# Kernel optimization log

Hardware: AMD Instinct MI355X
Metric: run time of the kernel (lower is better)

## Reference

```python
import jax, jax.numpy as jnp
import numpy as np

D_MODEL = 1024
NUM_HEADS = 16
D_K = D_MODEL // NUM_HEADS
B, S = 2, 2048


def setup_inputs() -> dict:
    key = jax.random.key(0)
    ks = jax.random.split(key, 12)
    s = 1.0 / np.sqrt(D_MODEL)
    return {
        "query": jax.random.normal(ks[0], (B, S, D_MODEL), jnp.float32),
        "key": jax.random.normal(ks[1], (B, S, D_MODEL), jnp.float32),
        "value": jax.random.normal(ks[2], (B, S, D_MODEL), jnp.float32),
        "mask": jnp.ones((B, S), jnp.int32),
        "Wq": jax.random.uniform(ks[3], (D_MODEL, D_MODEL), jnp.float32, -s, s),
        "bq": jax.random.uniform(ks[4], (D_MODEL,), jnp.float32, -s, s),
        "Wk": jax.random.uniform(ks[5], (D_MODEL, D_MODEL), jnp.float32, -s, s),
        "bk": jax.random.uniform(ks[6], (D_MODEL,), jnp.float32, -s, s),
        "Wv": jax.random.uniform(ks[7], (D_MODEL, D_MODEL), jnp.float32, -s, s),
        "bv": jax.random.uniform(ks[8], (D_MODEL,), jnp.float32, -s, s),
        "Wo": jax.random.uniform(ks[9], (D_MODEL, D_MODEL), jnp.float32, -s, s),
        "bo": jax.random.uniform(ks[10], (D_MODEL,), jnp.float32, -s, s),
    }


def reference(query, key, value, mask, Wq, bq, Wk, bk, Wv, bv, Wo, bo):
    b, s, _ = query.shape
    scale = jnp.sqrt(jnp.asarray(D_K, jnp.float32)).astype(query.dtype)
    # QKV projections: x @ W.T + b (torch nn.Linear convention)
    Q = (query @ Wq.T + bq).reshape(b, s, NUM_HEADS, D_K).transpose(0, 2, 1, 3)
    K = (key @ Wk.T + bk).reshape(b, -1, NUM_HEADS, D_K).transpose(0, 2, 1, 3)
    V = (value @ Wv.T + bv).reshape(b, -1, NUM_HEADS, D_K).transpose(0, 2, 1, 3)
    # scores in fp32, then cast back to input dtype (matches source)
    scores = jnp.einsum('bhqd,bhkd->bhqk', Q.astype(jnp.float32), K.astype(jnp.float32)) / scale
    scores = scores.astype(Q.dtype)
    # 2D mask [B,S] -> [B,1,1,S], broadcast over heads/queries
    fill = jnp.finfo(scores.dtype).min
    scores = jnp.where(mask[:, None, None, :] == 0, fill, scores)
    attn = jax.nn.softmax(scores, axis=-1)  # dropout p=0 -> identity
    context = jnp.einsum('bhqk,bhkd->bhqd', attn, V)
    context = context.transpose(0, 2, 1, 3).reshape(b, s, D_MODEL)
    return context @ Wo.T + bo
```

## Files before the change

### kernel.cpp

```cpp
#include <hip/hip_runtime.h>


typedef __bf16 bf16_8 __attribute__((ext_vector_type(8)));
typedef float  f32x4  __attribute__((ext_vector_type(4)));

#define MFMA16(a, b, c) __builtin_amdgcn_mfma_f32_16x16x32_bf16((a), (b), (c), 0, 0, 0)

__device__ __forceinline__ void async_ld16(const void* g, void* l) {
  __builtin_amdgcn_global_load_lds(
      (__attribute__((address_space(1))) void*)g,
      (__attribute__((address_space(3))) void*)l, 16, 0, 0);
}

__device__ __forceinline__ void gemm_core_128(
    const __bf16* __restrict__ A, const __bf16* __restrict__ BT, int K,
    int tm, int tn, __bf16* At, __bf16* Bt, f32x4 acc[4][4]) {
  const int tid  = threadIdx.x;
  const int lane = tid & 63;
  const int w    = tid >> 6;
  const int quad = lane >> 4;
  const int c16  = lane & 15;
  const int wm = w >> 1, wn = w & 1;

  const int ch0  = w * 2;
  const int row0 = ch0 * 16 + (lane >> 2);
  const int col0 = (lane & 3) * 8;
  const __bf16* Ag = A  + (size_t)(tm + row0) * K + col0;
  const __bf16* Bg = BT + (size_t)(tn + row0) * K + col0;
  __bf16* Al = At + ch0 * 512;
  __bf16* Bl = Bt + ch0 * 512;
  const size_t rowK16 = (size_t)16 * K;

  for (int kt = 0; kt < K; kt += 32) {
    async_ld16(Ag + kt,          Al);
    async_ld16(Ag + rowK16 + kt, Al + 512);
    async_ld16(Bg + kt,          Bl);
    async_ld16(Bg + rowK16 + kt, Bl + 512);
    __syncthreads();

    bf16_8 af[4], bfr[4];
#pragma unroll
    for (int mi = 0; mi < 4; ++mi)
      af[mi] = *(const bf16_8*)(At + (wm * 64 + mi * 16 + c16) * 32 + quad * 8);
#pragma unroll
    for (int ni = 0; ni < 4; ++ni)
      bfr[ni] = *(const bf16_8*)(Bt + (wn * 64 + ni * 16 + c16) * 32 + quad * 8);
#pragma unroll
    for (int mi = 0; mi < 4; ++mi)
#pragma unroll
      for (int ni = 0; ni < 4; ++ni)
        acc[mi][ni] = MFMA16(af[mi], bfr[ni], acc[mi][ni]);
    __syncthreads();
  }
}

__global__ __launch_bounds__(256)
void qkv_fused(const __bf16* __restrict__ xq, const __bf16* __restrict__ xk,
               const __bf16* __restrict__ xv,
               const __bf16* __restrict__ wq, const __bf16* __restrict__ wk,
               const __bf16* __restrict__ wv,
               const float* __restrict__ bq, const float* __restrict__ bk,
               const float* __restrict__ bv,
               __bf16* __restrict__ Qo, __bf16* __restrict__ Ko,
               __bf16* __restrict__ Vo) {
  __shared__ __bf16 At[128 * 32];
  __shared__ __bf16 Bt[128 * 32];
  const int z  = blockIdx.z;
  const int bx = blockIdx.x;
  const __bf16 *A, *BT;
  const float* bias;
  int tm, tn;
  if (z == 2) {
    A = wv; BT = xv; bias = bv;
    tm = (bx >> 5) * 128; tn = (bx & 31) * 128;
  } else if (z == 1) {
    A = xk; BT = wk; bias = bk;
    tm = (bx >> 3) * 128; tn = (bx & 7) * 128;
  } else {
    A = xq; BT = wq; bias = bq;
    tm = (bx >> 3) * 128; tn = (bx & 7) * 128;
  }

  f32x4 acc[4][4];
  const f32x4 zero4 = {0.f, 0.f, 0.f, 0.f};
#pragma unroll
  for (int i = 0; i < 4; ++i)
#pragma unroll
    for (int j = 0; j < 4; ++j) acc[i][j] = zero4;

  gemm_core_128(A, BT, 1024, tm, tn, At, Bt, acc);

  const int lane = threadIdx.x & 63;
  const int w    = threadIdx.x >> 6;
  const int quad = lane >> 4, c16 = lane & 15;
  const int wm = w >> 1, wn = w & 1;

  if (z == 2) {
#pragma unroll
    for (int mi = 0; mi < 4; ++mi) {
#pragma unroll
      for (int ni = 0; ni < 4; ++ni) {
        const int n  = tn + wn * 64 + ni * 16 + c16;
        const int bb = n >> 11, s = n & 2047;
#pragma unroll
        for (int r = 0; r < 4; ++r) {
          const int m  = tm + wm * 64 + mi * 16 + quad * 4 + r;
          const int hh = m >> 6, d = m & 63;
          Vo[(((size_t)(bb * 16 + hh) * 64 + d) << 11) + s] =
              (__bf16)(acc[mi][ni][r] + bias[m]);
        }
      }
    }
  } else {
    __bf16* Out = (z == 1) ? Ko : Qo;
    const float scale = (z == 0) ? 0.125f : 1.0f;
#pragma unroll
    for (int mi = 0; mi < 4; ++mi) {
#pragma unroll
      for (int ni = 0; ni < 4; ++ni) {
        const int n  = tn + wn * 64 + ni * 16 + c16;
        const int hh = n >> 6, d = n & 63;
        const float bn = bias[n];
#pragma unroll
        for (int r = 0; r < 4; ++r) {
          const int m  = tm + wm * 64 + mi * 16 + quad * 4 + r;
          const int bb = m >> 11, s = m & 2047;
          Out[(((size_t)(bb * 16 + hh) * 2048 + s) << 6) + d] =
              (__bf16)((acc[mi][ni][r] + bn) * scale);
        }
      }
    }
  }
}

__global__ __launch_bounds__(256)
void out_proj(const __bf16* __restrict__ ctx, const __bf16* __restrict__ wo,
              const float* __restrict__ bo, float* __restrict__ out) {
  __shared__ __bf16 At[64 * 32];
  __shared__ __bf16 Bt[128 * 32];
  const int bx = blockIdx.x;
  const int tm = (bx >> 3) * 64, tn = (bx & 7) * 128;

  const int tid  = threadIdx.x;
  const int lane = tid & 63, w = tid >> 6;
  const int quad = lane >> 4, c16 = lane & 15;
  const int wm = w >> 1, wn = w & 1;

  const int row0 = lane >> 2, col0 = (lane & 3) * 8;
  const __bf16* Ag = ctx + (size_t)(tm + w * 16 + row0) * 1024 + col0;
  const __bf16* Bg = wo  + (size_t)(tn + w * 32 + row0) * 1024 + col0;
  __bf16* Al = At + w * 512;
  __bf16* Bl = Bt + w * 1024;

  f32x4 acc[2][4];
  const f32x4 zero4 = {0.f, 0.f, 0.f, 0.f};
#pragma unroll
  for (int i = 0; i < 2; ++i)
#pragma unroll
    for (int j = 0; j < 4; ++j) acc[i][j] = zero4;

  for (int kt = 0; kt < 1024; kt += 32) {
    async_ld16(Ag + kt, Al);
    async_ld16(Bg + kt, Bl);
    async_ld16(Bg + 16 * 1024 + kt, Bl + 512);
    __syncthreads();

    bf16_8 af[2], bfr[4];
#pragma unroll
    for (int mi = 0; mi < 2; ++mi)
      af[mi] = *(const bf16_8*)(At + (wm * 32 + mi * 16 + c16) * 32 + quad * 8);
#pragma unroll
    for (int ni = 0; ni < 4; ++ni)
      bfr[ni] = *(const bf16_8*)(Bt + (wn * 64 + ni * 16 + c16) * 32 + quad * 8);
#pragma unroll
    for (int mi = 0; mi < 2; ++mi)
#pragma unroll
      for (int ni = 0; ni < 4; ++ni)
        acc[mi][ni] = MFMA16(af[mi], bfr[ni], acc[mi][ni]);
    __syncthreads();
  }

#pragma unroll
  for (int mi = 0; mi < 2; ++mi) {
#pragma unroll
    for (int ni = 0; ni < 4; ++ni) {
      const int n = tn + wn * 64 + ni * 16 + c16;
      const float bn = bo[n];
#pragma unroll
      for (int r = 0; r < 4; ++r) {
        const int m = tm + wm * 32 + mi * 16 + quad * 4 + r;
        out[(size_t)m * 1024 + n] = acc[mi][ni][r] + bn;
      }
    }
  }
}

__global__ __launch_bounds__(256)
void flash_attn(const __bf16* __restrict__ Qg, const __bf16* __restrict__ Kg,
                const __bf16* __restrict__ VTg, const int* __restrict__ maskg,
                __bf16* __restrict__ ctx) {
  __shared__ __bf16 Kl[64 * 72];
  __shared__ __bf16 Vl[64 * 72];
  __shared__ __bf16 Pl[128 * 72];
  __shared__ float  maskadd[64];

  const int t    = threadIdx.x;
  const int lane = t & 63, w = t >> 6;
  const int quad = lane >> 4, c16 = lane & 15;
  const int qt = blockIdx.x, h = blockIdx.y, b = blockIdx.z;
  const size_t bh = (size_t)(b * 16 + h);
  const int qbase = qt * 128 + w * 32;

  bf16_8 aq[2][2];
#pragma unroll
  for (int mi = 0; mi < 2; ++mi) {
    const __bf16* qptr = Qg + (bh * 2048 + qbase + mi * 16 + c16) * 64;
    aq[mi][0] = *(const bf16_8*)(qptr + quad * 8);
    aq[mi][1] = *(const bf16_8*)(qptr + 32 + quad * 8);
  }

  f32x4 o[2][4];
  const f32x4 zero4 = {0.f, 0.f, 0.f, 0.f};
#pragma unroll
  for (int mi = 0; mi < 2; ++mi)
#pragma unroll
    for (int dt = 0; dt < 4; ++dt) o[mi][dt] = zero4;
  float lsum[2][4] = {{0.f, 0.f, 0.f, 0.f}, {0.f, 0.f, 0.f, 0.f}};

  const int srow = t >> 2;
  const int scc  = (t & 3) * 16;
  const __bf16* Kgp = Kg + bh * 2048 * 64;
  const __bf16* Vgp = VTg + bh * 64 * 2048;
  const float LOG2E = 1.44269504088896f;

  for (int kt = 0; kt < 2048; kt += 64) {
    {
      const size_t kb = (size_t)(kt + srow) * 64 + scc;
      *(bf16_8*)&Kl[srow * 72 + scc]     = *(const bf16_8*)&Kgp[kb];
      *(bf16_8*)&Kl[srow * 72 + scc + 8] = *(const bf16_8*)&Kgp[kb + 8];
      const size_t vb = (size_t)srow * 2048 + kt + scc;
      *(bf16_8*)&Vl[srow * 72 + scc]     = *(const bf16_8*)&Vgp[vb];
      *(bf16_8*)&Vl[srow * 72 + scc + 8] = *(const bf16_8*)&Vgp[vb + 8];
      if (t < 64) maskadd[t] = maskg[b * 2048 + kt + t] ? -17.3123404907f : -1e30f;
    }
    __syncthreads();

#pragma unroll
    for (int nt = 0; nt < 4; ++nt) {
      const bf16_8 b0 = *(const bf16_8*)&Kl[(nt * 16 + c16) * 72 + quad * 8];
      const bf16_8 b1 = *(const bf16_8*)&Kl[(nt * 16 + c16) * 72 + 32 + quad * 8];
      const float ma = maskadd[nt * 16 + c16];
#pragma unroll
      for (int mi = 0; mi < 2; ++mi) {
        f32x4 sf = MFMA16(aq[mi][1], b1, MFMA16(aq[mi][0], b0, zero4));
#pragma unroll
        for (int r = 0; r < 4; ++r) {
          const float p = __builtin_amdgcn_exp2f(fmaf(sf[r], LOG2E, ma));
          lsum[mi][r] += p;
          Pl[(w * 32 + mi * 16 + quad * 4 + r) * 72 + nt * 16 + c16] = (__bf16)p;
        }
      }
    }

#pragma unroll
    for (int kf = 0; kf < 2; ++kf) {
      const bf16_8 pa0 = *(const bf16_8*)&Pl[(w * 32 + c16) * 72 + kf * 32 + quad * 8];
      const bf16_8 pa1 = *(const bf16_8*)&Pl[(w * 32 + 16 + c16) * 72 + kf * 32 + quad * 8];
#pragma unroll
      for (int dt = 0; dt < 4; ++dt) {
        const bf16_8 vb = *(const bf16_8*)&Vl[(dt * 16 + c16) * 72 + kf * 32 + quad * 8];
        o[0][dt] = MFMA16(pa0, vb, o[0][dt]);
        o[1][dt] = MFMA16(pa1, vb, o[1][dt]);
      }
    }
    __syncthreads();
  }

#pragma unroll
  for (int mi = 0; mi < 2; ++mi)
#pragma unroll
    for (int r = 0; r < 4; ++r) {
      float rs = lsum[mi][r];
      rs += __shfl_xor(rs, 1);
      rs += __shfl_xor(rs, 2);
      rs += __shfl_xor(rs, 4);
      rs += __shfl_xor(rs, 8);
      lsum[mi][r] = 1.0f / rs;
    }

#pragma unroll
  for (int mi = 0; mi < 2; ++mi) {
    const int sbase = qbase + mi * 16 + quad * 4;
#pragma unroll
    for (int dt = 0; dt < 4; ++dt) {
#pragma unroll
      for (int r = 0; r < 4; ++r) {
        ctx[((size_t)b * 2048 + sbase + r) * 1024 + h * 64 + dt * 16 + c16] =
            (__bf16)(o[mi][dt][r] * lsum[mi][r]);
      }
    }
  }
}

__global__ __launch_bounds__(256)
void cvt_all(const float* __restrict__ q, const float* __restrict__ k,
             const float* __restrict__ v, const float* __restrict__ Wq,
             const float* __restrict__ Wk, const float* __restrict__ Wv,
             const float* __restrict__ Wo,
             __bf16* __restrict__ xq, __bf16* __restrict__ xk,
             __bf16* __restrict__ xv, __bf16* __restrict__ wqb,
             __bf16* __restrict__ wkb, __bf16* __restrict__ wvb,
             __bf16* __restrict__ wob) {
  const int y = blockIdx.y;
  const float* s;
  __bf16* d;
  int n8;
  switch (y) {
    case 0: s = q;  d = xq;  n8 = 524288; break;
    case 1: s = k;  d = xk;  n8 = 524288; break;
    case 2: s = v;  d = xv;  n8 = 524288; break;
    case 3: s = Wq; d = wqb; n8 = 131072; break;
    case 4: s = Wk; d = wkb; n8 = 131072; break;
    case 5: s = Wv; d = wvb; n8 = 131072; break;
    default: s = Wo; d = wob; n8 = 131072; break;
  }
  const int i = blockIdx.x * blockDim.x + threadIdx.x;
  if (i < n8) {
    const float4* sp = (const float4*)s;
    const float4 v0 = sp[i * 2], v1 = sp[i * 2 + 1];
    bf16_8 o;
    o[0] = (__bf16)v0.x; o[1] = (__bf16)v0.y;
    o[2] = (__bf16)v0.z; o[3] = (__bf16)v0.w;
    o[4] = (__bf16)v1.x; o[5] = (__bf16)v1.y;
    o[6] = (__bf16)v1.z; o[7] = (__bf16)v1.w;
    *(bf16_8*)(d + (size_t)i * 8) = o;
  }
}

extern "C" void kernel_launch(void* const* d_in, const int* in_sizes, int n_in,
                              void* d_out, int out_size, void* d_ws, size_t ws_size,
                              hipStream_t stream) {
  (void)in_sizes; (void)n_in; (void)out_size; (void)ws_size;
  const float* q    = (const float*)d_in[0];
  const float* k    = (const float*)d_in[1];
  const float* v    = (const float*)d_in[2];
  const int*   mask = (const int*)d_in[3];
  const float* Wq = (const float*)d_in[4];
  const float* bq = (const float*)d_in[5];
  const float* Wk = (const float*)d_in[6];
  const float* bk = (const float*)d_in[7];
  const float* Wv = (const float*)d_in[8];
  const float* bv = (const float*)d_in[9];
  const float* Wo = (const float*)d_in[10];
  const float* bo = (const float*)d_in[11];

  char* ws = (char*)d_ws;
  const size_t MB = 1ull << 20;
  __bf16* xq  = (__bf16*)(ws + 0 * MB);
  __bf16* xk  = (__bf16*)(ws + 8 * MB);
  __bf16* xv  = (__bf16*)(ws + 16 * MB);
  __bf16* wqb = (__bf16*)(ws + 24 * MB);
  __bf16* wkb = (__bf16*)(ws + 26 * MB);
  __bf16* wvb = (__bf16*)(ws + 28 * MB);
  __bf16* wob = (__bf16*)(ws + 30 * MB);
  __bf16* Qb  = (__bf16*)(ws + 32 * MB);
  __bf16* Kb  = (__bf16*)(ws + 40 * MB);
  __bf16* VTb = (__bf16*)(ws + 48 * MB);
  __bf16* ctx = (__bf16*)(ws + 56 * MB);

  cvt_all<<<dim3(2048, 7), 256, 0, stream>>>(q, k, v, Wq, Wk, Wv, Wo,
                                             xq, xk, xv, wqb, wkb, wvb, wob);

  qkv_fused<<<dim3(256, 1, 3), 256, 0, stream>>>(xq, xk, xv, wqb, wkb, wvb,
                                                 bq, bk, bv, Qb, Kb, VTb);

  flash_attn<<<dim3(16, 16, 2), 256, 0, stream>>>(Qb, Kb, VTb, mask, ctx);

  out_proj<<<dim3(512), 256, 0, stream>>>(ctx, wob, bo, (float*)d_out);
}
```

Before: 249.8 us.

## Keep P in registers for flash attention using transposed MFMA and swizzled LDS

The attention kernel now computes S transposed (K as the A operand), so the exp'd probabilities come out in registers in the layout the 16x16x16 bf16 MFMA B-operand expects. This removes the LDS round trip for P and its extra writes and reads. K/V tiles are stored with an XOR swizzle instead of padding. The block shrinks to 128 threads covering 64 queries, with twice as many blocks, and the output is staged through LDS so global stores are coalesced 16-byte writes. The risk is that the smaller-K MFMA halves work per instruction, and the added MFMA builtin fallback paths may not match the hardware.

```diff
diff --git a/kernel.cpp b/kernel.cpp
--- a/kernel.cpp
+++ b/kernel.cpp
@@ -2,9 +2,26 @@
 
 
 typedef __bf16 bf16_8 __attribute__((ext_vector_type(8)));
+typedef __bf16 bf16_4 __attribute__((ext_vector_type(4)));
 typedef float  f32x4  __attribute__((ext_vector_type(4)));
 
 #define MFMA16(a, b, c) __builtin_amdgcn_mfma_f32_16x16x32_bf16((a), (b), (c), 0, 0, 0)
+
+#if __has_builtin(__builtin_amdgcn_mfma_f32_16x16x16_bf16)
+#define MFMA_PV(a, b, c) __builtin_amdgcn_mfma_f32_16x16x16_bf16((a), (b), (c), 0, 0, 0)
+#elif __has_builtin(__builtin_amdgcn_mfma_f32_16x16x16bf16_1k)
+typedef short s16x4 __attribute__((ext_vector_type(4)));
+#define MFMA_PV(a, b, c)                                                  \
+  __builtin_amdgcn_mfma_f32_16x16x16bf16_1k(                              \
+      __builtin_bit_cast(s16x4, (a)), __builtin_bit_cast(s16x4, (b)), (c), 0, 0, 0)
+#else
+static __device__ __forceinline__ f32x4 mfma_pv_asm(bf16_4 a, bf16_4 b, f32x4 c) {
+  asm volatile("v_mfma_f32_16x16x16_bf16 %0, %1, %2, %0\n\ts_nop 3"
+               : "+v"(c) : "v"(a), "v"(b));
+  return c;
+}
+#define MFMA_PV(a, b, c) mfma_pv_asm((a), (b), (c))
+#endif
 
 __device__ __forceinline__ void async_ld16(const void* g, void* l) {
   __builtin_amdgcn_global_load_lds(
@@ -195,21 +212,22 @@
   }
 }
 
-__global__ __launch_bounds__(256)
+__global__ __launch_bounds__(128)
 void flash_attn(const __bf16* __restrict__ Qg, const __bf16* __restrict__ Kg,
                 const __bf16* __restrict__ VTg, const int* __restrict__ maskg,
                 __bf16* __restrict__ ctx) {
-  __shared__ __bf16 Kl[64 * 72];
-  __shared__ __bf16 Vl[64 * 72];
-  __shared__ __bf16 Pl[128 * 72];
-  __shared__ float  maskadd[64];
+  __shared__ __bf16 KV[8192];
+  __shared__ alignas(16) float maskadd[64];
+  __bf16* Kl = KV;
+  __bf16* Vl = KV + 4096;
 
   const int t    = threadIdx.x;
   const int lane = t & 63, w = t >> 6;
   const int quad = lane >> 4, c16 = lane & 15;
+  const int sw   = c16 & 7;
   const int qt = blockIdx.x, h = blockIdx.y, b = blockIdx.z;
   const size_t bh = (size_t)(b * 16 + h);
-  const int qbase = qt * 128 + w * 32;
+  const int qbase = qt * 64 + w * 32;
 
   bf16_8 aq[2][2];
 #pragma unroll
@@ -219,87 +237,89 @@
     aq[mi][1] = *(const bf16_8*)(qptr + 32 + quad * 8);
   }
 
-  f32x4 o[2][4];
+  f32x4 o[4][2];
   const f32x4 zero4 = {0.f, 0.f, 0.f, 0.f};
 #pragma unroll
-  for (int mi = 0; mi < 2; ++mi)
-#pragma unroll
-    for (int dt = 0; dt < 4; ++dt) o[mi][dt] = zero4;
-  float lsum[2][4] = {{0.f, 0.f, 0.f, 0.f}, {0.f, 0.f, 0.f, 0.f}};
-
-  const int srow = t >> 2;
-  const int scc  = (t & 3) * 16;
+  for (int dt = 0; dt < 4; ++dt)
+#pragma unroll
+    for (int mi = 0; mi < 2; ++mi) o[dt][mi] = zero4;
+  float lsum[2] = {0.f, 0.f};
+
   const __bf16* Kgp = Kg + bh * 2048 * 64;
   const __bf16* Vgp = VTg + bh * 64 * 2048;
-  const float LOG2E = 1.44269504088896f;
+  const float LOG2E  = 1.44269504088896f;
+  const float SHIFT2 = -17.3123404907f;
 
   for (int kt = 0; kt < 2048; kt += 64) {
-    {
-      const size_t kb = (size_t)(kt + srow) * 64 + scc;
-      *(bf16_8*)&Kl[srow * 72 + scc]     = *(const bf16_8*)&Kgp[kb];
-      *(bf16_8*)&Kl[srow * 72 + scc + 8] = *(const bf16_8*)&Kgp[kb + 8];
-      const size_t vb = (size_t)srow * 2048 + kt + scc;
-      *(bf16_8*)&Vl[srow * 72 + scc]     = *(const bf16_8*)&Vgp[vb];
-      *(bf16_8*)&Vl[srow * 72 + scc + 8] = *(const bf16_8*)&Vgp[vb + 8];
-      if (t < 64) maskadd[t] = maskg[b * 2048 + kt + t] ? -17.3123404907f : -1e30f;
+#pragma unroll
+    for (int i = 0; i < 4; ++i) {
+      const int c = t * 4 + i;
+      const int row = c >> 3, ch = c & 7;
+      const int dst = row * 64 + (((ch ^ (row & 7))) << 3);
+      *(bf16_8*)&Kl[dst] = *(const bf16_8*)&Kgp[(size_t)(kt + row) * 64 + (ch << 3)];
+      *(bf16_8*)&Vl[dst] = *(const bf16_8*)&Vgp[(size_t)row * 2048 + kt + (ch << 3)];
     }
-    __syncthreads();
-
-#pragma unroll
-    for (int nt = 0; nt < 4; ++nt) {
-      const bf16_8 b0 = *(const bf16_8*)&Kl[(nt * 16 + c16) * 72 + quad * 8];
-      const bf16_8 b1 = *(const bf16_8*)&Kl[(nt * 16 + c16) * 72 + 32 + quad * 8];
-      const float ma = maskadd[nt * 16 + c16];
+    if (t < 64) maskadd[t] = maskg[b * 2048 + kt + t] ? SHIFT2 : -1e30f;
+    __syncthreads();
+
+#pragma unroll
+    for (int kb = 0; kb < 4; ++kb) {
+      const int krow = (kb * 16 + c16) * 64;
+      const bf16_8 kf0 = *(const bf16_8*)&Kl[krow + ((quad ^ sw) << 3)];
+      const bf16_8 kf1 = *(const bf16_8*)&Kl[krow + (((quad + 4) ^ sw) << 3)];
+      const f32x4 mav = ((const f32x4*)maskadd)[kb * 4 + quad];
+
+      bf16_4 pf[2];
 #pragma unroll
       for (int mi = 0; mi < 2; ++mi) {
-        f32x4 sf = MFMA16(aq[mi][1], b1, MFMA16(aq[mi][0], b0, zero4));
-#pragma unroll
-        for (int r = 0; r < 4; ++r) {
-          const float p = __builtin_amdgcn_exp2f(fmaf(sf[r], LOG2E, ma));
-          lsum[mi][r] += p;
-          Pl[(w * 32 + mi * 16 + quad * 4 + r) * 72 + nt * 16 + c16] = (__bf16)p;
-        }
+        f32x4 sf = MFMA16(kf1, aq[mi][1], MFMA16(kf0, aq[mi][0], zero4));
+        const float p0 = __builtin_amdgcn_exp2f(fmaf(sf[0], LOG2E, mav[0]));
+        const float p1 = __builtin_amdgcn_exp2f(fmaf(sf[1], LOG2E, mav[1]));
+        const float p2 = __builtin_amdgcn_exp2f(fmaf(sf[2], LOG2E, mav[2]));
+        const float p3 = __builtin_amdgcn_exp2f(fmaf(sf[3], LOG2E, mav[3]));
+        lsum[mi] += (p0 + p1) + (p2 + p3);
+        bf16_4 pp = {(__bf16)p0, (__bf16)p1, (__bf16)p2, (__bf16)p3};
+        pf[mi] = pp;
+      }
+
+#pragma unroll
+      for (int dt = 0; dt < 4; ++dt) {
+        const int drow = (dt * 16 + c16) * 64;
+        const bf16_4 vf = *(const bf16_4*)&Vl[drow +
+            (((2 * kb + (quad >> 1)) ^ sw) << 3) + ((quad & 1) << 2)];
+        o[dt][0] = MFMA_PV(vf, pf[0], o[dt][0]);
+        o[dt][1] = MFMA_PV(vf, pf[1], o[dt][1]);
       }
     }
-
-#pragma unroll
-    for (int kf = 0; kf < 2; ++kf) {
-      const bf16_8 pa0 = *(const bf16_8*)&Pl[(w * 32 + c16) * 72 + kf * 32 + quad * 8];
-      const bf16_8 pa1 = *(const bf16_8*)&Pl[(w * 32 + 16 + c16) * 72 + kf * 32 + quad * 8];
-#pragma unroll
-      for (int dt = 0; dt < 4; ++dt) {
-        const bf16_8 vb = *(const bf16_8*)&Vl[(dt * 16 + c16) * 72 + kf * 32 + quad * 8];
-        o[0][dt] = MFMA16(pa0, vb, o[0][dt]);
-        o[1][dt] = MFMA16(pa1, vb, o[1][dt]);
-      }
-    }
-    __syncthreads();
-  }
-
-#pragma unroll
-  for (int mi = 0; mi < 2; ++mi)
-#pragma unroll
-    for (int r = 0; r < 4; ++r) {
-      float rs = lsum[mi][r];
-      rs += __shfl_xor(rs, 1);
-      rs += __shfl_xor(rs, 2);
-      rs += __shfl_xor(rs, 4);
-      rs += __shfl_xor(rs, 8);
-      lsum[mi][r] = 1.0f / rs;
-    }
-
+    __syncthreads();
+  }
+
+  float rl[2];
 #pragma unroll
   for (int mi = 0; mi < 2; ++mi) {
-    const int sbase = qbase + mi * 16 + quad * 4;
-#pragma unroll
-    for (int dt = 0; dt < 4; ++dt) {
-#pragma unroll
-      for (int r = 0; r < 4; ++r) {
-        ctx[((size_t)b * 2048 + sbase + r) * 1024 + h * 64 + dt * 16 + c16] =
-            (__bf16)(o[mi][dt][r] * lsum[mi][r]);
-      }
-    }
-  }
+    float s_ = lsum[mi];
+    s_ += __shfl_xor(s_, 16);
+    s_ += __shfl_xor(s_, 32);
+    rl[mi] = 1.0f / s_;
+  }
+
+  __bf16* Oe = KV + w * 2304;
+#pragma unroll
+  for (int dt = 0; dt < 4; ++dt)
+#pragma unroll
+    for (int mi = 0; mi < 2; ++mi)
+#pragma unroll
+      for (int r = 0; r < 4; ++r)
+        Oe[(mi * 16 + c16) * 72 + dt * 16 + quad * 4 + r] =
+            (__bf16)(o[dt][mi][r] * rl[mi]);
+  __syncthreads();
+
+  const int rq = lane >> 1, hf = lane & 1;
+  const __bf16* src = KV + w * 2304 + rq * 72 + hf * 32;
+  __bf16* dst = ctx + ((size_t)b * 2048 + qbase + rq) * 1024 + h * 64 + hf * 32;
+#pragma unroll
+  for (int j = 0; j < 4; ++j)
+    *(bf16_8*)(dst + j * 8) = *(const bf16_8*)(src + j * 8);
 }
 
 __global__ __launch_bounds__(256)
@@ -374,7 +394,7 @@
   qkv_fused<<<dim3(256, 1, 3), 256, 0, stream>>>(xq, xk, xv, wqb, wkb, wvb,
                                                  bq, bk, bv, Qb, Kb, VTb);
 
-  flash_attn<<<dim3(16, 16, 2), 256, 0, stream>>>(Qb, Kb, VTb, mask, ctx);
+  flash_attn<<<dim3(32, 16, 2), 128, 0, stream>>>(Qb, Kb, VTb, mask, ctx);
 
   out_proj<<<dim3(512), 256, 0, stream>>>(ctx, wob, bo, (float*)d_out);
 }
```

Measured after the change: 282.8 us. +13.2%, slower.
